# Kernel tuning notes

Hardware: AMD Instinct MI355X
Metric: run time of the kernel (lower is better)

## Reference

```python
import jax, jax.numpy as jnp
import numpy as np

T, B, D, H = 1024, 256, 128, 256

def setup_inputs() -> dict:
    key = jax.random.key(0)
    ks = jax.random.split(key, 6)
    s = 1.0 / np.sqrt(H)
    return {
        "x": jax.random.normal(ks[0], (T, B, D), dtype=jnp.float32),
        "delta_ts": jax.random.uniform(ks[1], (B, T), dtype=jnp.float32) * 10.0,  # elapsed times > 0
        "h0": jnp.zeros((B, H), dtype=jnp.float32),
        "c0": jnp.zeros((B, H), dtype=jnp.float32),
        "W": jax.random.normal(ks[2], (4 * H, D), dtype=jnp.float32) * s,
        "U": jax.random.normal(ks[3], (4 * H, H), dtype=jnp.float32) * s,
        "b": jnp.zeros((4 * H,), dtype=jnp.float32),
        "Wd": jax.random.normal(ks[4], (H, H), dtype=jnp.float32) * s,
        "bd": jnp.zeros((H,), dtype=jnp.float32),
    }

def reference(x, delta_ts, h0, c0, W, U, b, Wd, bd):
    """Time-aware LSTM (T-LSTM, Baytas et al. 2017) layer over time-major input.
    x: [T,B,D], delta_ts: [B,T]. Returns (outputs [T,B,H], (h,c))."""
    e = jnp.float32(np.e)

    def step(carry, inp):
        h, c = carry                 # [B,H] each
        xt, dt = inp                 # [B,D], [B]
        # memory decomposition with elapsed-time discount g(dt)=1/log(e+dt)
        Cs = jnp.tanh(c @ Wd.T + bd)                     # short-term memory [B,H]
        Cs_hat = Cs * (1.0 / jnp.log(e + dt))[:, None]   # discounted short-term
        c_star = c - Cs + Cs_hat                          # adjusted previous cell
        gates = xt @ W.T + h @ U.T + b                    # [B,4H]
        i, f, g, o = jnp.split(gates, 4, axis=-1)
        c_new = jax.nn.sigmoid(f) * c_star + jax.nn.sigmoid(i) * jnp.tanh(g)
        h_new = jax.nn.sigmoid(o) * jnp.tanh(c_new)
        return (h_new, c_new), h_new

    (h, c), outs = jax.lax.scan(step, (h0, c0), (x, delta_ts.T))
    return outs, h, c
```

## Files before the change

### kernel.cpp

```cpp
#include <hip/hip_runtime.h>

#define T_STEPS 1024
#define BATCH   256
#define DIM     128
#define HID     256
#define NSLICE  8
#define BT      16
#define NGROUP  (BATCH / BT)
#define NBLOCK  (NGROUP * NSLICE)
#define JW      (HID / NSLICE)

#define U_OFF    0
#define W_OFF    65536
#define WD_OFF   98304
#define H_OFF    114688
#define C_OFF    122880
#define GST_OFF  131072
#define CST_OFF  139520
#define SMEM_TOTAL 141632

typedef float f32x4 __attribute__((ext_vector_type(4)));
typedef short bf16x8 __attribute__((ext_vector_type(8)));

__device__ __forceinline__ unsigned short f2bf(float f) {
    union { float f; unsigned u; } v; v.f = f;
    unsigned r = (v.u + 0x7fffu + ((v.u >> 16) & 1u)) >> 16;
    return (unsigned short)r;
}
__device__ __forceinline__ float sigm(float v) { return 1.0f / (1.0f + __expf(-v)); }
__device__ __forceinline__ float tanh_fast(float v) {
    const float e = __expf(2.0f * v);
    return 1.0f - 2.0f / (e + 1.0f);
}

__global__ __launch_bounds__(512)
void tlstm_kernel(const float* __restrict__ x,
                  const float* __restrict__ dts,
                  const float* __restrict__ h0,
                  const float* __restrict__ c0,
                  const float* __restrict__ W,
                  const float* __restrict__ U,
                  const float* __restrict__ bvec,
                  const float* __restrict__ Wd,
                  const float* __restrict__ bd,
                  float* __restrict__ out,
                  unsigned int* ctr,
                  unsigned long long* hbuf,
                  unsigned long long* cbuf)
{
    extern __shared__ char smem[];
    float* gates_st = (float*)(smem + GST_OFF);
    float* cs_st    = (float*)(smem + CST_OFF);

    const int tid = threadIdx.x;
    const int g  = blockIdx.x / NSLICE;
    const int s  = blockIdx.x % NSLICE;
    const int bb = g * BT;
    const int jb = s * JW;

    const int lane = tid & 63;
    const int wid  = tid >> 6;
    const int lrow = lane & 15;
    const int lkg  = lane >> 4;
    const int n0   = wid << 4;

    const int b_ = tid >> 5;
    const int jj = tid & 31;

    for (int idx = tid; idx < 128 * 256; idx += 512) {
        const int r = idx >> 8, k = idx & 255;
        const int urow = ((r >> 5) * HID) + jb + (r & 31);
        int bo = (r << 9) + (k << 1); bo ^= (r & 7) << 4;
        *(unsigned short*)(smem + U_OFF + bo) = f2bf(U[(size_t)urow * HID + k]);
    }
    for (int idx = tid; idx < 128 * 128; idx += 512) {
        const int r = idx >> 7, k = idx & 127;
        const int wrow = ((r >> 5) * HID) + jb + (r & 31);
        int bo = (r << 8) + (k << 1); bo ^= (r & 7) << 4;
        *(unsigned short*)(smem + W_OFF + bo) = f2bf(W[(size_t)wrow * DIM + k]);
    }
    for (int idx = tid; idx < 32 * 256; idx += 512) {
        const int r = idx >> 8, k = idx & 255;
        int bo = (r << 9) + (k << 1); bo ^= (r & 7) << 4;
        *(unsigned short*)(smem + WD_OFF + bo) = f2bf(Wd[(size_t)(jb + r) * HID + k]);
    }

    const float bI = bvec[jb + jj];
    const float bF = bvec[HID + jb + jj];
    const float bG = bvec[2 * HID + jb + jj];
    const float bO = bvec[3 * HID + jb + jj];
    const float bD = bd[jb + jj];

    float4 xr[8];
    float dt_cur;
    {
        const float* xp = x + ((size_t)0 * BATCH + bb + lrow) * DIM + (lkg << 3);
        #pragma unroll
        for (int kc = 0; kc < 4; ++kc) {
            xr[2 * kc]     = *(const float4*)(xp + kc * 32);
            xr[2 * kc + 1] = *(const float4*)(xp + kc * 32 + 4);
        }
        dt_cur = dts[(size_t)(bb + b_) * T_STEPS + 0];
    }

    float c_reg;
    {
        const float h0v = h0[(size_t)(bb + b_) * HID + jb + jj];
        const float c0v = c0[(size_t)(bb + b_) * HID + jb + jj];
        c_reg = c0v;
        const unsigned short hb16 = f2bf(h0v), cb16 = f2bf(c0v);
        const int oh = __shfl_xor((int)hb16, 1);
        const int oc = __shfl_xor((int)cb16, 1);
        if ((jj & 1) == 0) {
            const unsigned int hw = (unsigned)hb16 | ((unsigned)oh << 16);
            const unsigned int cw = (unsigned)cb16 | ((unsigned)oc << 16);
            const size_t ei = ((size_t)(bb + b_) * HID + jb + jj) >> 1;
            __hip_atomic_store((unsigned int*)hbuf + ei, hw, __ATOMIC_RELAXED, __HIP_MEMORY_SCOPE_AGENT);
            __hip_atomic_store((unsigned int*)cbuf + ei, cw, __ATOMIC_RELAXED, __HIP_MEMORY_SCOPE_AGENT);
        }
    }
    __syncthreads();
    if (tid == 0)
        __hip_atomic_fetch_add(&ctr[g << 5], 1u, __ATOMIC_RELAXED, __HIP_MEMORY_SCOPE_AGENT);
    if (lane == 0) {
        while (__hip_atomic_load(&ctr[g << 5], __ATOMIC_RELAXED, __HIP_MEMORY_SCOPE_AGENT)
               < (unsigned)NSLICE) {}
    }

    float hn_keep = 0.0f;

    for (int t = 0; t < T_STEPS; ++t) {
        const int cur = t & 1;
        const unsigned long long* hsrc = hbuf + (size_t)cur * (BATCH * HID / 4);
        const unsigned long long* csrc = cbuf + (size_t)cur * (BATCH * HID / 4);

        #pragma unroll
        for (int rep = 0; rep < 2; ++rep) {
            const int idx = tid + rep * 512;
            const int row = idx >> 6, qk = idx & 63;
            const unsigned long long hq = __hip_atomic_load(
                (unsigned long long*)(hsrc + (size_t)(bb + row) * (HID / 4) + qk),
                __ATOMIC_RELAXED, __HIP_MEMORY_SCOPE_AGENT);
            const unsigned long long cq = __hip_atomic_load(
                (unsigned long long*)(csrc + (size_t)(bb + row) * (HID / 4) + qk),
                __ATOMIC_RELAXED, __HIP_MEMORY_SCOPE_AGENT);
            int bo = (row << 9) + (qk << 3); bo ^= (row & 7) << 4;
            *(unsigned long long*)(smem + H_OFF + bo) = hq;
            *(unsigned long long*)(smem + C_OFF + bo) = cq;
        }

        if (t > 0)
            out[((size_t)(t - 1) * BATCH + bb + b_) * HID + jb + jj] = hn_keep;

        bf16x8 xa[4];
        #pragma unroll
        for (int kc = 0; kc < 4; ++kc) {
            const float4 f0 = xr[2 * kc];
            const float4 f1 = xr[2 * kc + 1];
            bf16x8 a;
            a[0] = (short)f2bf(f0.x); a[1] = (short)f2bf(f0.y);
            a[2] = (short)f2bf(f0.z); a[3] = (short)f2bf(f0.w);
            a[4] = (short)f2bf(f1.x); a[5] = (short)f2bf(f1.y);
            a[6] = (short)f2bf(f1.z); a[7] = (short)f2bf(f1.w);
            xa[kc] = a;
        }
        __syncthreads();

        f32x4 accX = {0.f, 0.f, 0.f, 0.f};
        f32x4 accH = {0.f, 0.f, 0.f, 0.f};
        {
            const int wr = n0 + lrow;
            #pragma unroll
            for (int kc = 0; kc < 4; ++kc) {
                int wo = (wr << 8) + ((kc * 32 + (lkg << 3)) << 1); wo ^= (wr & 7) << 4;
                const bf16x8 wv = *(const bf16x8*)(smem + W_OFF + wo);
                accX = __builtin_amdgcn_mfma_f32_16x16x32_bf16(xa[kc], wv, accX, 0, 0, 0);
            }
            #pragma unroll
            for (int kc = 0; kc < 8; ++kc) {
                int ao = (lrow << 9) + ((kc * 32 + (lkg << 3)) << 1); ao ^= (lrow & 7) << 4;
                const bf16x8 av = *(const bf16x8*)(smem + H_OFF + ao);
                int uo = (wr << 9) + ((kc * 32 + (lkg << 3)) << 1); uo ^= (wr & 7) << 4;
                const bf16x8 uv = *(const bf16x8*)(smem + U_OFF + uo);
                accH = __builtin_amdgcn_mfma_f32_16x16x32_bf16(av, uv, accH, 0, 0, 0);
            }
        }
        if (wid < 2) {
            f32x4 accC = {0.f, 0.f, 0.f, 0.f};
            const int wr = (wid << 4) + lrow;
            #pragma unroll
            for (int kc = 0; kc < 8; ++kc) {
                int ao = (lrow << 9) + ((kc * 32 + (lkg << 3)) << 1); ao ^= (lrow & 7) << 4;
                const bf16x8 av = *(const bf16x8*)(smem + C_OFF + ao);
                int wo = (wr << 9) + ((kc * 32 + (lkg << 3)) << 1); wo ^= (wr & 7) << 4;
                const bf16x8 wv = *(const bf16x8*)(smem + WD_OFF + wo);
                accC = __builtin_amdgcn_mfma_f32_16x16x32_bf16(av, wv, accC, 0, 0, 0);
            }
            #pragma unroll
            for (int i = 0; i < 4; ++i)
                cs_st[((lkg << 2) + i) * 33 + (wid << 4) + lrow] = accC[i];
        }
        #pragma unroll
        for (int i = 0; i < 4; ++i)
            gates_st[((lkg << 2) + i) * 132 + n0 + lrow] = accX[i] + accH[i];

        __syncthreads();

        float cn, hn;
        {
            const float ipre = gates_st[b_ * 132 + jj]      + bI;
            const float fpre = gates_st[b_ * 132 + 32 + jj] + bF;
            const float gpre = gates_st[b_ * 132 + 64 + jj] + bG;
            const float opre = gates_st[b_ * 132 + 96 + jj] + bO;
            const float cspre = cs_st[b_ * 33 + jj] + bD;
            const float gdt  = 1.0f / __logf(2.718281828459045f + dt_cur);
            const float Cs    = tanh_fast(cspre);
            const float cstar = c_reg - Cs + Cs * gdt;
            cn = sigm(fpre) * cstar + sigm(ipre) * tanh_fast(gpre);
            hn = sigm(opre) * tanh_fast(cn);
            c_reg = cn;
            hn_keep = hn;
        }

        if (t == T_STEPS - 1) {
            out[((size_t)t * BATCH + bb + b_) * HID + jb + jj] = hn;
            const size_t base = (size_t)T_STEPS * BATCH * HID;
            out[base + (size_t)(bb + b_) * HID + jb + jj] = hn;
            out[base + (size_t)BATCH * HID + (size_t)(bb + b_) * HID + jb + jj] = cn;
            break;
        }

        {
            const unsigned short hb16 = f2bf(hn), cb16 = f2bf(cn);
            const int oh = __shfl_xor((int)hb16, 1);
            const int oc = __shfl_xor((int)cb16, 1);
            if ((jj & 1) == 0) {
                const unsigned int hw = (unsigned)hb16 | ((unsigned)oh << 16);
                const unsigned int cw = (unsigned)cb16 | ((unsigned)oc << 16);
                const size_t ei = (size_t)(cur ^ 1) * (BATCH * HID / 2)
                                + (((size_t)(bb + b_) * HID + jb + jj) >> 1);
                __hip_atomic_store((unsigned int*)hbuf + ei, hw, __ATOMIC_RELAXED, __HIP_MEMORY_SCOPE_AGENT);
                __hip_atomic_store((unsigned int*)cbuf + ei, cw, __ATOMIC_RELAXED, __HIP_MEMORY_SCOPE_AGENT);
            }
        }
        __syncthreads();

        if (tid == 0)
            __hip_atomic_fetch_add(&ctr[g << 5], 1u, __ATOMIC_RELAXED, __HIP_MEMORY_SCOPE_AGENT);
        {
            const float* xp = x + ((size_t)(t + 1) * BATCH + bb + lrow) * DIM + (lkg << 3);
            #pragma unroll
            for (int kc = 0; kc < 4; ++kc) {
                xr[2 * kc]     = *(const float4*)(xp + kc * 32);
                xr[2 * kc + 1] = *(const float4*)(xp + kc * 32 + 4);
            }
            dt_cur = dts[(size_t)(bb + b_) * T_STEPS + (t + 1)];
        }
        {
            const unsigned target = (unsigned)(NSLICE * (t + 2));
            if (lane == 0) {
                while (__hip_atomic_load(&ctr[g << 5], __ATOMIC_RELAXED, __HIP_MEMORY_SCOPE_AGENT)
                       < target) {}
            }
        }
    }
}

extern "C" void kernel_launch(void* const* d_in, const int* in_sizes, int n_in,
                              void* d_out, int out_size, void* d_ws, size_t ws_size,
                              hipStream_t stream) {
    (void)in_sizes; (void)n_in; (void)out_size; (void)ws_size;
    const float* x   = (const float*)d_in[0];
    const float* dts = (const float*)d_in[1];
    const float* h0  = (const float*)d_in[2];
    const float* c0  = (const float*)d_in[3];
    const float* W   = (const float*)d_in[4];
    const float* U   = (const float*)d_in[5];
    const float* bv  = (const float*)d_in[6];
    const float* Wd  = (const float*)d_in[7];
    const float* bd  = (const float*)d_in[8];
    float* out = (float*)d_out;

    char* ws = (char*)d_ws;
    unsigned int*       ctr  = (unsigned int*)ws;
    unsigned long long* hbuf = (unsigned long long*)(ws + 4096);
    unsigned long long* cbuf = (unsigned long long*)(ws + 4096 + 262144);

    hipMemsetAsync(ctr, 0, NGROUP * 32 * sizeof(unsigned int), stream);
    hipFuncSetAttribute((const void*)tlstm_kernel,
                        hipFuncAttributeMaxDynamicSharedMemorySize, SMEM_TOTAL);
    tlstm_kernel<<<dim3(NBLOCK), dim3(512), SMEM_TOTAL, stream>>>(
        x, dts, h0, c0, W, U, bv, Wd, bd, out, ctr, hbuf, cbuf);
}
```

Before: 4.660 ms.

## Replace group barrier with per-wave flags and overlap x-projection with wait

The shared per-group atomic counter and block-wide barrier are replaced by per-wave, per-slice flag words. Each wave waits only for the 8 flags of the slice whose h/c data it consumes, then loads that slice from a repacked contiguous buffer. The x·W MFMA now runs before the wait so it overlaps the cross-block latency, and the Wd·c product is split across 4 waves with a K-split reduction. The risks are finer-grained memory-ordering assumptions (relaxed stores plus s_waitcnt) and more flag polling traffic.

```diff
diff --git a/kernel.cpp b/kernel.cpp
--- a/kernel.cpp
+++ b/kernel.cpp
@@ -16,8 +16,9 @@
 #define H_OFF    114688
 #define C_OFF    122880
 #define GST_OFF  131072
-#define CST_OFF  139520
-#define SMEM_TOTAL 141632
+#define CS0_OFF  139520
+#define CS1_OFF  141632
+#define SMEM_TOTAL 143744
 
 typedef float f32x4 __attribute__((ext_vector_type(4)));
 typedef short bf16x8 __attribute__((ext_vector_type(8)));
@@ -32,6 +33,8 @@
     const float e = __expf(2.0f * v);
     return 1.0f - 2.0f / (e + 1.0f);
 }
+
+#define FLAG_IDX(g, s, w) (((g) * 8 + (s)) * 32 + (w))
 
 __global__ __launch_bounds__(512)
 void tlstm_kernel(const float* __restrict__ x,
@@ -44,13 +47,14 @@
                   const float* __restrict__ Wd,
                   const float* __restrict__ bd,
                   float* __restrict__ out,
-                  unsigned int* ctr,
-                  unsigned long long* hbuf,
-                  unsigned long long* cbuf)
+                  unsigned int* flags,
+                  unsigned int* hb32,
+                  unsigned int* cb32)
 {
     extern __shared__ char smem[];
     float* gates_st = (float*)(smem + GST_OFF);
-    float* cs_st    = (float*)(smem + CST_OFF);
+    float* cs0      = (float*)(smem + CS0_OFF);
+    float* cs1      = (float*)(smem + CS1_OFF);
 
     const int tid = threadIdx.x;
     const int g  = blockIdx.x / NSLICE;
@@ -114,43 +118,18 @@
         if ((jj & 1) == 0) {
             const unsigned int hw = (unsigned)hb16 | ((unsigned)oh << 16);
             const unsigned int cw = (unsigned)cb16 | ((unsigned)oc << 16);
-            const size_t ei = ((size_t)(bb + b_) * HID + jb + jj) >> 1;
-            __hip_atomic_store((unsigned int*)hbuf + ei, hw, __ATOMIC_RELAXED, __HIP_MEMORY_SCOPE_AGENT);
-            __hip_atomic_store((unsigned int*)cbuf + ei, cw, __ATOMIC_RELAXED, __HIP_MEMORY_SCOPE_AGENT);
-        }
-    }
-    __syncthreads();
-    if (tid == 0)
-        __hip_atomic_fetch_add(&ctr[g << 5], 1u, __ATOMIC_RELAXED, __HIP_MEMORY_SCOPE_AGENT);
-    if (lane == 0) {
-        while (__hip_atomic_load(&ctr[g << 5], __ATOMIC_RELAXED, __HIP_MEMORY_SCOPE_AGENT)
-               < (unsigned)NSLICE) {}
-    }
-
-    float hn_keep = 0.0f;
+            const int ei = (((0 * NGROUP + g) * 8 + s) * 16 + b_) * 16 + (jj >> 1);
+            __hip_atomic_store(hb32 + ei, hw, __ATOMIC_RELAXED, __HIP_MEMORY_SCOPE_AGENT);
+            __hip_atomic_store(cb32 + ei, cw, __ATOMIC_RELAXED, __HIP_MEMORY_SCOPE_AGENT);
+        }
+    }
+    asm volatile("s_waitcnt vmcnt(0)" ::: "memory");
+    if (lane == 0)
+        __hip_atomic_store(flags + FLAG_IDX(g, s, wid), 1u,
+                           __ATOMIC_RELAXED, __HIP_MEMORY_SCOPE_AGENT);
 
     for (int t = 0; t < T_STEPS; ++t) {
         const int cur = t & 1;
-        const unsigned long long* hsrc = hbuf + (size_t)cur * (BATCH * HID / 4);
-        const unsigned long long* csrc = cbuf + (size_t)cur * (BATCH * HID / 4);
-
-        #pragma unroll
-        for (int rep = 0; rep < 2; ++rep) {
-            const int idx = tid + rep * 512;
-            const int row = idx >> 6, qk = idx & 63;
-            const unsigned long long hq = __hip_atomic_load(
-                (unsigned long long*)(hsrc + (size_t)(bb + row) * (HID / 4) + qk),
-                __ATOMIC_RELAXED, __HIP_MEMORY_SCOPE_AGENT);
-            const unsigned long long cq = __hip_atomic_load(
-                (unsigned long long*)(csrc + (size_t)(bb + row) * (HID / 4) + qk),
-                __ATOMIC_RELAXED, __HIP_MEMORY_SCOPE_AGENT);
-            int bo = (row << 9) + (qk << 3); bo ^= (row & 7) << 4;
-            *(unsigned long long*)(smem + H_OFF + bo) = hq;
-            *(unsigned long long*)(smem + C_OFF + bo) = cq;
-        }
-
-        if (t > 0)
-            out[((size_t)(t - 1) * BATCH + bb + b_) * HID + jb + jj] = hn_keep;
 
         bf16x8 xa[4];
         #pragma unroll
@@ -164,10 +143,7 @@
             a[6] = (short)f2bf(f1.z); a[7] = (short)f2bf(f1.w);
             xa[kc] = a;
         }
-        __syncthreads();
-
         f32x4 accX = {0.f, 0.f, 0.f, 0.f};
-        f32x4 accH = {0.f, 0.f, 0.f, 0.f};
         {
             const int wr = n0 + lrow;
             #pragma unroll
@@ -176,6 +152,42 @@
                 const bf16x8 wv = *(const bf16x8*)(smem + W_OFF + wo);
                 accX = __builtin_amdgcn_mfma_f32_16x16x32_bf16(xa[kc], wv, accX, 0, 0, 0);
             }
+        }
+
+        {
+            const unsigned target = (unsigned)(t + 1);
+            const unsigned* fb = flags + FLAG_IDX(g, wid, 0);
+            unsigned fl = target;
+            do {
+                if (lane < 8)
+                    fl = __hip_atomic_load(fb + lane, __ATOMIC_RELAXED, __HIP_MEMORY_SCOPE_AGENT);
+            } while (__any((int)(fl < target)));
+        }
+        asm volatile("" ::: "memory");
+        __builtin_amdgcn_sched_barrier(0);
+
+        {
+            const int boff = ((cur * NGROUP + g) * 8 + wid) * 256;
+            const unsigned long long* hq = (const unsigned long long*)(hb32 + boff);
+            const unsigned long long* cq = (const unsigned long long*)(cb32 + boff);
+            const unsigned long long h1 = __hip_atomic_load(hq + lane,      __ATOMIC_RELAXED, __HIP_MEMORY_SCOPE_AGENT);
+            const unsigned long long h2 = __hip_atomic_load(hq + lane + 64, __ATOMIC_RELAXED, __HIP_MEMORY_SCOPE_AGENT);
+            const unsigned long long c1 = __hip_atomic_load(cq + lane,      __ATOMIC_RELAXED, __HIP_MEMORY_SCOPE_AGENT);
+            const unsigned long long c2 = __hip_atomic_load(cq + lane + 64, __ATOMIC_RELAXED, __HIP_MEMORY_SCOPE_AGENT);
+            const int r1 = lane >> 3, r2 = 8 + (lane >> 3);
+            const int cb = (wid << 6) + ((lane & 7) << 3);
+            int bo1 = (r1 << 9) + cb; bo1 ^= (r1 & 7) << 4;
+            int bo2 = (r2 << 9) + cb; bo2 ^= (r2 & 7) << 4;
+            *(unsigned long long*)(smem + H_OFF + bo1) = h1;
+            *(unsigned long long*)(smem + H_OFF + bo2) = h2;
+            *(unsigned long long*)(smem + C_OFF + bo1) = c1;
+            *(unsigned long long*)(smem + C_OFF + bo2) = c2;
+        }
+        __syncthreads();
+
+        f32x4 accH = {0.f, 0.f, 0.f, 0.f};
+        {
+            const int wr = n0 + lrow;
             #pragma unroll
             for (int kc = 0; kc < 8; ++kc) {
                 int ao = (lrow << 9) + ((kc * 32 + (lkg << 3)) << 1); ao ^= (lrow & 7) << 4;
@@ -185,20 +197,24 @@
                 accH = __builtin_amdgcn_mfma_f32_16x16x32_bf16(av, uv, accH, 0, 0, 0);
             }
         }
-        if (wid < 2) {
+        if (wid < 4) {
             f32x4 accC = {0.f, 0.f, 0.f, 0.f};
-            const int wr = (wid << 4) + lrow;
-            #pragma unroll
-            for (int kc = 0; kc < 8; ++kc) {
-                int ao = (lrow << 9) + ((kc * 32 + (lkg << 3)) << 1); ao ^= (lrow & 7) << 4;
+            const int nt = wid >> 1;
+            const int kh = wid & 1;
+            const int wr = (nt << 4) + lrow;
+            #pragma unroll
+            for (int kc = 0; kc < 4; ++kc) {
+                const int kk = kh * 4 + kc;
+                int ao = (lrow << 9) + ((kk * 32 + (lkg << 3)) << 1); ao ^= (lrow & 7) << 4;
                 const bf16x8 av = *(const bf16x8*)(smem + C_OFF + ao);
-                int wo = (wr << 9) + ((kc * 32 + (lkg << 3)) << 1); wo ^= (wr & 7) << 4;
+                int wo = (wr << 9) + ((kk * 32 + (lkg << 3)) << 1); wo ^= (wr & 7) << 4;
                 const bf16x8 wv = *(const bf16x8*)(smem + WD_OFF + wo);
                 accC = __builtin_amdgcn_mfma_f32_16x16x32_bf16(av, wv, accC, 0, 0, 0);
             }
+            float* dst = kh ? cs1 : cs0;
             #pragma unroll
             for (int i = 0; i < 4; ++i)
-                cs_st[((lkg << 2) + i) * 33 + (wid << 4) + lrow] = accC[i];
+                dst[((lkg << 2) + i) * 33 + (nt << 4) + lrow] = accC[i];
         }
         #pragma unroll
         for (int i = 0; i < 4; ++i)
@@ -212,14 +228,13 @@
             const float fpre = gates_st[b_ * 132 + 32 + jj] + bF;
             const float gpre = gates_st[b_ * 132 + 64 + jj] + bG;
             const float opre = gates_st[b_ * 132 + 96 + jj] + bO;
-            const float cspre = cs_st[b_ * 33 + jj] + bD;
+            const float cspre = cs0[b_ * 33 + jj] + cs1[b_ * 33 + jj] + bD;
             const float gdt  = 1.0f / __logf(2.718281828459045f + dt_cur);
             const float Cs    = tanh_fast(cspre);
             const float cstar = c_reg - Cs + Cs * gdt;
             cn = sigm(fpre) * cstar + sigm(ipre) * tanh_fast(gpre);
             hn = sigm(opre) * tanh_fast(cn);
             c_reg = cn;
-            hn_keep = hn;
         }
 
         if (t == T_STEPS - 1) {
@@ -237,16 +252,17 @@
             if ((jj & 1) == 0) {
                 const unsigned int hw = (unsigned)hb16 | ((unsigned)oh << 16);
                 const unsigned int cw = (unsigned)cb16 | ((unsigned)oc << 16);
-                const size_t ei = (size_t)(cur ^ 1) * (BATCH * HID / 2)
-                                + (((size_t)(bb + b_) * HID + jb + jj) >> 1);
-                __hip_atomic_store((unsigned int*)hbuf + ei, hw, __ATOMIC_RELAXED, __HIP_MEMORY_SCOPE_AGENT);
-                __hip_atomic_store((unsigned int*)cbuf + ei, cw, __ATOMIC_RELAXED, __HIP_MEMORY_SCOPE_AGENT);
-            }
-        }
-        __syncthreads();
-
-        if (tid == 0)
-            __hip_atomic_fetch_add(&ctr[g << 5], 1u, __ATOMIC_RELAXED, __HIP_MEMORY_SCOPE_AGENT);
+                const int ei = ((((cur ^ 1) * NGROUP + g) * 8 + s) * 16 + b_) * 16 + (jj >> 1);
+                __hip_atomic_store(hb32 + ei, hw, __ATOMIC_RELAXED, __HIP_MEMORY_SCOPE_AGENT);
+                __hip_atomic_store(cb32 + ei, cw, __ATOMIC_RELAXED, __HIP_MEMORY_SCOPE_AGENT);
+            }
+        }
+        asm volatile("s_waitcnt vmcnt(0)" ::: "memory");
+        if (lane == 0)
+            __hip_atomic_store(flags + FLAG_IDX(g, s, wid), (unsigned)(t + 2),
+                               __ATOMIC_RELAXED, __HIP_MEMORY_SCOPE_AGENT);
+
+        out[((size_t)t * BATCH + bb + b_) * HID + jb + jj] = hn;
         {
             const float* xp = x + ((size_t)(t + 1) * BATCH + bb + lrow) * DIM + (lkg << 3);
             #pragma unroll
@@ -255,13 +271,6 @@
                 xr[2 * kc + 1] = *(const float4*)(xp + kc * 32 + 4);
             }
             dt_cur = dts[(size_t)(bb + b_) * T_STEPS + (t + 1)];
-        }
-        {
-            const unsigned target = (unsigned)(NSLICE * (t + 2));
-            if (lane == 0) {
-                while (__hip_atomic_load(&ctr[g << 5], __ATOMIC_RELAXED, __HIP_MEMORY_SCOPE_AGENT)
-                       < target) {}
-            }
         }
     }
 }
@@ -282,13 +291,13 @@
     float* out = (float*)d_out;
 
     char* ws = (char*)d_ws;
-    unsigned int*       ctr  = (unsigned int*)ws;
-    unsigned long long* hbuf = (unsigned long long*)(ws + 4096);
-    unsigned long long* cbuf = (unsigned long long*)(ws + 4096 + 262144);
-
-    hipMemsetAsync(ctr, 0, NGROUP * 32 * sizeof(unsigned int), stream);
+    unsigned int* flags = (unsigned int*)ws;
+    unsigned int* hb32  = (unsigned int*)(ws + 16384);
+    unsigned int* cb32  = (unsigned int*)(ws + 16384 + 262144);
+
+    hipMemsetAsync(flags, 0, 16384, stream);
     hipFuncSetAttribute((const void*)tlstm_kernel,
                         hipFuncAttributeMaxDynamicSharedMemorySize, SMEM_TOTAL);
     tlstm_kernel<<<dim3(NBLOCK), dim3(512), SMEM_TOTAL, stream>>>(
-        x, dts, h0, c0, W, U, bv, Wd, bd, out, ctr, hbuf, cbuf);
+        x, dts, h0, c0, W, U, bv, Wd, bd, out, flags, hb32, cb32);
 }
```

New measurement: 4.821 ms. 1.03x slower.
